# Kernel tuning notes

Measured on AMD Instinct MI355X. Metric: run time of the kernel, lower is better.

The kernel has to match this reference:

```python
import jax, jax.numpy as jnp
import numpy as np
from jax import lax

S = 262144   # sequence length (dim 2)
D = 16       # embedding width (dim 3)
L = 20       # number of conv layers
K_TOP = 800


def _conv(x, w, b, pad):
    # x: [B,C,H,W], w: [O,I,kh,1]; conv along H with symmetric padding, stride 1
    y = lax.conv_general_dilated(x, w, (1, 1), [(pad, pad), (0, 0)],
                                 dimension_numbers=('NCHW', 'OIHW', 'NCHW'))
    return y + b[None, :, None, None]


def _fold(x):
    # Faithful to the torch fold(): pairwise sum along width (dim 3), then the
    # buggy concatenation of C copies along dim 2 and B copies along dim 1.
    B, C, H, W = x.shape
    c = x[..., 0::2] + x[..., 1::2]          # [B,C,H,W//2]
    b = jnp.concatenate([c] * C, axis=2)      # [B,C,H*C,W//2]
    return jnp.concatenate([b] * B, axis=1)   # [B,C*B,H*C,W//2]


def _kmax(x, k):
    # torch k_max_pool returns top-k along dim 2 (H) for every width column
    # (the outer loops are dead code: it returns the last inner result `c`).
    xt = jnp.swapaxes(x, 2, 3)                # [B,C,W,H]
    v = lax.top_k(xt, k)[0]                   # [B,C,W,k] (descending)
    return jnp.swapaxes(v, 2, 3)              # [B,C,k,W]


def _prelu(x, a):
    return jnp.where(x >= 0, x, a * x)


def _forward(x, w0, b0, wm, bm, w18, b18, w19, b19, a1, a2, Wfc, bfc):
    s = x.shape[2]
    # layer 0: conv(99) -> fold -> kmax(max(k_top, s)) -> PReLU1
    h = _prelu(_kmax(_fold(_conv(x, w0, b0, 98)), max(K_TOP, s)), a1)
    # layers 1..17: conv(9) -> kmax -> PReLU2 (layer 1) / ReLU (layers 2..17)
    for i in range(17):
        k = max(K_TOP, int((L - 1 - i) / float(L) * s))
        h = _conv(h, wm[i], bm[i], 8)
        h = _kmax(h, k)
        h = _prelu(h, a2) if i == 0 else jax.nn.relu(h)
    # layer 18: conv(9) -> fold -> kmax -> ELU
    k18 = max(K_TOP, int((L - 18) / float(L) * s))
    h = jax.nn.elu(_kmax(_fold(_conv(h, w18, b18, 8)), k18))
    # layer 19: conv(358) -> fold -> kmax(k_top) -> ELU
    h = jax.nn.elu(_kmax(_fold(_conv(h, w19, b19, 357)), K_TOP))   # [1,5,800,2]
    h = h.reshape(-1, 2 * K_TOP)              # [5, 1600]
    h = h @ Wfc.T + bfc                        # dropout in eval = identity
    h = h.reshape(1, -1)                       # [1, 1000]; log_softmax dim=len(x)=1
    return jax.nn.log_softmax(h, axis=1)


def setup_inputs() -> dict:
    key = jax.random.key(0)
    ks = jax.random.split(key, 12)
    n = lambda k, sh, sc: jax.random.normal(k, sh, jnp.float32) * sc
    return {
        'x':   n(ks[0], (1, 1, S, D), 1.0),
        'w0':  n(ks[1], (2, 1, 99, 1), 0.05),  'b0':  n(ks[2], (2,), 0.05),
        'wm':  n(ks[3], (17, 2, 2, 9, 1), 0.2), 'bm': n(ks[4], (17, 2), 0.05),
        'w18': n(ks[5], (2, 2, 9, 1), 0.2),    'b18': n(ks[6], (2,), 0.05),
        'w19': n(ks[7], (5, 2, 358, 1), 0.03), 'b19': n(ks[8], (5,), 0.05),
        'a1': jnp.float32(0.25), 'a2': jnp.float32(0.25),
        'Wfc': n(ks[9], (200, 1600), 0.02),    'bfc': n(ks[10], (200,), 0.02),
    }


def reference(x, w0, b0, wm, bm, w18, b18, w19, b19, a1, a2, Wfc, bfc):
    return _forward(x, w0, b0, wm, bm, w18, b18, w19, b19, a1, a2, Wfc, bfc)
```

## Files before the change

### kernel.cpp

```cpp
#include <hip/hip_runtime.h>
#include <math.h>

typedef unsigned int u32;
typedef unsigned long long u64;

#define STRIDE 262656
#define KSHIFT 15
#define KROUND 0x4000u
#define BAND   6144
#define NB     12288
#define PA17   0x7100u
#define NA17   0x17700u
#define NCOLS  16
#define ZW     (NB*NCOLS)
#define ACT_PRELU 0
#define ACT_RELU  1
#define ACT_ELU   2

__device__ __forceinline__ float k2f(u32 k){
    u32 u = (k & 0x80000000u) ? k : (k ^ 0x7FFFFFFFu);
    return __uint_as_float(u);
}
__device__ __forceinline__ int bin_of(float v){
    float av = fabsf(v);
    av = fminf(fmaxf(av, 0.00390625f), 65535.96875f);
    u32 u = __float_as_uint(av);
    if (v < 0.f){
        u32 k = 0x80000000u | u;
        int b = (int)(((k + KROUND) >> KSHIFT) - NA17);
        b = b < 0 ? 0 : (b > BAND-1 ? BAND-1 : b);
        return BAND + b;
    } else {
        u32 k = u ^ 0x7FFFFFFFu;
        int b = (int)(((k + KROUND) >> KSHIFT) - PA17);
        b = b < 0 ? 0 : (b > BAND-1 ? BAND-1 : b);
        return b;
    }
}
__device__ __forceinline__ float bin_val(int bin){
    u32 k17 = (bin < BAND) ? ((u32)bin + PA17) : ((u32)(bin - BAND) + NA17);
    return k2f(k17 << KSHIFT);
}

__device__ __forceinline__ void hist_add(u32* __restrict__ Hc, int bin, bool valid, int lane){
    u32 bn = valid ? (u32)bin : 0xFFFFFFFFu;
    u32 prev = __shfl_up(bn, 1);
    bool diff = (lane == 0) || (prev != bn);
    u64 m = __ballot(diff || !valid);
    if (valid && diff){
        u64 above = m & ~((2ull << lane) - 1ull);
        int nxt = above ? (__ffsll((unsigned long long)above) - 1) : 64;
        atomicAdd(&Hc[bin], (u32)(nxt - lane));
    }
}

__device__ __forceinline__ void lds_hist_dedup(u32* __restrict__ hist, int bin, bool valid, int lane){
    u32 bn = valid ? (u32)bin : 0xFFFFFFFFu;
    u32 prev = __shfl_up(bn, 1);
    bool diff = (lane == 0) || (prev != bn);
    u64 m = __ballot(diff || !valid);
    if (valid && diff){
        u64 above = m & ~((2ull << lane) - 1ull);
        int nxt = above ? (__ffsll((unsigned long long)above) - 1) : 64;
        u32 cnt = (u32)(nxt - lane);
        atomicAdd(&hist[bin >> 1], cnt << ((bin & 1) * 16));
    }
}

__global__ __launch_bounds__(256) void foldx(const float* __restrict__ x, float* __restrict__ fx,
                                             uint4* __restrict__ zb)
{
    __shared__ float4 tile[1024];
    const int tid = threadIdx.x;
    const int h0 = blockIdx.x * 256;
    for (int i = tid; i < 1024; i += 256) tile[i] = ((const float4*)x)[(size_t)h0*4 + i];
    __syncthreads();
    float4 a = tile[tid*4+0], b = tile[tid*4+1], c = tile[tid*4+2], d = tile[tid*4+3];
    const int h = h0 + tid;
    fx[(size_t)0*STRIDE + h] = a.x + a.y;
    fx[(size_t)1*STRIDE + h] = a.z + a.w;
    fx[(size_t)2*STRIDE + h] = b.x + b.y;
    fx[(size_t)3*STRIDE + h] = b.z + b.w;
    fx[(size_t)4*STRIDE + h] = c.x + c.y;
    fx[(size_t)5*STRIDE + h] = c.z + c.w;
    fx[(size_t)6*STRIDE + h] = d.x + d.y;
    fx[(size_t)7*STRIDE + h] = d.z + d.w;
    const uint4 z = make_uint4(0,0,0,0);
    for (int i = blockIdx.x*256 + tid; i < ZW/4; i += gridDim.x*256) zb[i] = z;
}

#define C0CHUNK 8192
__global__ __launch_bounds__(512) void conv0_lds(const float* __restrict__ fx, u32* __restrict__ H,
                                                 const float* __restrict__ w0, const float* __restrict__ b0)
{
    __shared__ u32 hist[NB/2];
    __shared__ __align__(16) float s0f[2148];
    __shared__ float sw[100];
    const int colv = blockIdx.y;
    const int o = colv >> 3, wp = colv & 7;
    const int tid = threadIdx.x;
    const int p0 = blockIdx.x * C0CHUNK;
    const int p1 = min(p0 + C0CHUNK, 262242);
    if (p0 >= 262242) return;
    for (int i = tid; i < NB/2; i += 512) hist[i] = 0;
    if (tid < 99) sw[tid] = w0[o*99 + tid];
    if (tid == 99) sw[99] = 0.f;
    const float bias = 2.f * b0[o];
    __syncthreads();
    const float* fc = fx + (size_t)wp * STRIDE;
    const float4* s4 = (const float4*)s0f;
    for (int t0 = p0; t0 < p1; t0 += 2048){
        for (int i = tid; i < 2148; i += 512){
            int h = t0 - 98 + i;
            s0f[i] = (h >= 0 && h < 262144) ? fc[h] : 0.f;
        }
        __syncthreads();
        float a0 = bias, a1 = bias, a2 = bias, a3 = bias;
        float4 c = s4[tid];
        #pragma unroll
        for (int jb = 0; jb < 25; jb++){
            float4 n = s4[tid + jb + 1];
            float w0_ = sw[4*jb+0], w1_ = sw[4*jb+1], w2_ = sw[4*jb+2], w3_ = sw[4*jb+3];
            a0 += w0_*c.x; a1 += w0_*c.y; a2 += w0_*c.z; a3 += w0_*c.w;
            a0 += w1_*c.y; a1 += w1_*c.z; a2 += w1_*c.w; a3 += w1_*n.x;
            a0 += w2_*c.z; a1 += w2_*c.w; a2 += w2_*n.x; a3 += w2_*n.y;
            a0 += w3_*c.w; a1 += w3_*n.x; a2 += w3_*n.y; a3 += w3_*n.z;
            c = n;
        }
        int hp = t0 + tid*4;
        if (hp     < p1){ int b = bin_of(a0); atomicAdd(&hist[b>>1], 1u << ((b&1)*16)); }
        if (hp + 1 < p1){ int b = bin_of(a1); atomicAdd(&hist[b>>1], 1u << ((b&1)*16)); }
        if (hp + 2 < p1){ int b = bin_of(a2); atomicAdd(&hist[b>>1], 1u << ((b&1)*16)); }
        if (hp + 3 < p1){ int b = bin_of(a3); atomicAdd(&hist[b>>1], 1u << ((b&1)*16)); }
        __syncthreads();
    }
    u32* Hc = H + (size_t)colv * NB;
    for (int i = tid; i < NB/2; i += 512){
        u32 w = hist[i];
        if (w){
            u32 lo = w & 0xFFFFu, hi = w >> 16;
            if (lo) atomicAdd(&Hc[2*i],   lo);
            if (hi) atomicAdd(&Hc[2*i+1], hi);
        }
    }
}

#define C9CHUNK 8192
template<int FOLDIN>
__global__ __launch_bounds__(512) void conv9_lds(
    const float* __restrict__ In, u32* __restrict__ H,
    const float* __restrict__ Wt, const float* __restrict__ Bs,
    int Hin, int Hout, int Wi, int Wo, float bscale)
{
    __shared__ u32 hist[NB/2];
    __shared__ __align__(16) float s0f[2056];
    __shared__ __align__(16) float s1f[2056];
    const int colv = blockIdx.y;
    const int o = colv / Wo, wp = colv % Wo;
    const int tid = threadIdx.x;
    const int lane = tid & 63;
    const int p0 = blockIdx.x * C9CHUNK;
    const int p1 = min(p0 + C9CHUNK, Hout);
    if (p0 >= Hout) return;
    for (int i = tid; i < NB/2; i += 512) hist[i] = 0;
    float w0r[9], w1r[9];
    #pragma unroll
    for (int j = 0; j < 9; j++){ w0r[j] = Wt[(o*2)*9 + j]; w1r[j] = Wt[(o*2)*9 + 9 + j]; }
    const float bv = bscale * Bs[o];
    __syncthreads();
    const float* i00 = In + (size_t)(0*Wi + (FOLDIN ? 2*wp   : wp))*STRIDE;
    const float* i01 = In + (size_t)(0*Wi + (FOLDIN ? 2*wp+1 : wp))*STRIDE;
    const float* i10 = In + (size_t)(1*Wi + (FOLDIN ? 2*wp   : wp))*STRIDE;
    const float* i11 = In + (size_t)(1*Wi + (FOLDIN ? 2*wp+1 : wp))*STRIDE;
    const float4* s40 = (const float4*)s0f;
    const float4* s41 = (const float4*)s1f;
    for (int t0 = p0; t0 < p1; t0 += 2048){
        for (int i = tid; i < 2056; i += 512){
            int h = t0 - 8 + i;
            float v0 = 0.f, v1 = 0.f;
            if (h >= 0 && h < Hin){
                v0 = FOLDIN ? (i00[h] + i01[h]) : i00[h];
                v1 = FOLDIN ? (i10[h] + i11[h]) : i10[h];
            }
            s0f[i] = v0; s1f[i] = v1;
        }
        __syncthreads();
        float a0 = bv, a1 = bv, a2 = bv, a3 = bv;
        {
            float4 X = s40[tid], Y = s40[tid+1], Z = s40[tid+2];
            a0 += w0r[0]*X.x; a1 += w0r[0]*X.y; a2 += w0r[0]*X.z; a3 += w0r[0]*X.w;
            a0 += w0r[1]*X.y; a1 += w0r[1]*X.z; a2 += w0r[1]*X.w; a3 += w0r[1]*Y.x;
            a0 += w0r[2]*X.z; a1 += w0r[2]*X.w; a2 += w0r[2]*Y.x; a3 += w0r[2]*Y.y;
            a0 += w0r[3]*X.w; a1 += w0r[3]*Y.x; a2 += w0r[3]*Y.y; a3 += w0r[3]*Y.z;
            a0 += w0r[4]*Y.x; a1 += w0r[4]*Y.y; a2 += w0r[4]*Y.z; a3 += w0r[4]*Y.w;
            a0 += w0r[5]*Y.y; a1 += w0r[5]*Y.z; a2 += w0r[5]*Y.w; a3 += w0r[5]*Z.x;
            a0 += w0r[6]*Y.z; a1 += w0r[6]*Y.w; a2 += w0r[6]*Z.x; a3 += w0r[6]*Z.y;
            a0 += w0r[7]*Y.w; a1 += w0r[7]*Z.x; a2 += w0r[7]*Z.y; a3 += w0r[7]*Z.z;
            a0 += w0r[8]*Z.x; a1 += w0r[8]*Z.y; a2 += w0r[8]*Z.z; a3 += w0r[8]*Z.w;
        }
        {
            float4 X = s41[tid], Y = s41[tid+1], Z = s41[tid+2];
            a0 += w1r[0]*X.x; a1 += w1r[0]*X.y; a2 += w1r[0]*X.z; a3 += w1r[0]*X.w;
            a0 += w1r[1]*X.y; a1 += w1r[1]*X.z; a2 += w1r[1]*X.w; a3 += w1r[1]*Y.x;
            a0 += w1r[2]*X.z; a1 += w1r[2]*X.w; a2 += w1r[2]*Y.x; a3 += w1r[2]*Y.y;
            a0 += w1r[3]*X.w; a1 += w1r[3]*Y.x; a2 += w1r[3]*Y.y; a3 += w1r[3]*Y.z;
            a0 += w1r[4]*Y.x; a1 += w1r[4]*Y.y; a2 += w1r[4]*Y.z; a3 += w1r[4]*Y.w;
            a0 += w1r[5]*Y.y; a1 += w1r[5]*Y.z; a2 += w1r[5]*Y.w; a3 += w1r[5]*Z.x;
            a0 += w1r[6]*Y.z; a1 += w1r[6]*Y.w; a2 += w1r[6]*Z.x; a3 += w1r[6]*Z.y;
            a0 += w1r[7]*Y.w; a1 += w1r[7]*Z.x; a2 += w1r[7]*Z.y; a3 += w1r[7]*Z.z;
            a0 += w1r[8]*Z.x; a1 += w1r[8]*Z.y; a2 += w1r[8]*Z.z; a3 += w1r[8]*Z.w;
        }
        int hp = t0 + tid*4;
        lds_hist_dedup(hist, bin_of(a0), hp     < p1, lane);
        lds_hist_dedup(hist, bin_of(a1), hp + 1 < p1, lane);
        lds_hist_dedup(hist, bin_of(a2), hp + 2 < p1, lane);
        lds_hist_dedup(hist, bin_of(a3), hp + 3 < p1, lane);
        __syncthreads();
    }
    u32* Hc = H + (size_t)colv * NB;
    for (int i = tid; i < NB/2; i += 512){
        u32 w = hist[i];
        if (w){
            u32 lo = w & 0xFFFFu, hi = w >> 16;
            if (lo) atomicAdd(&Hc[2*i],   lo);
            if (hi) atomicAdd(&Hc[2*i+1], hi);
        }
    }
}

template<int INC, int OUTC>
__global__ __launch_bounds__(256) void conv_hist_t(
    const float* __restrict__ In, u32* __restrict__ H,
    const float* __restrict__ Wt, const float* __restrict__ Bs,
    int Hin, int Hout, int K, int pad, int Wi, int Wo, int foldIn, float bscale)
{
    __shared__ float sIn[INC][613];
    __shared__ float sW[OUTC*INC*358];
    const int wp = blockIdx.y;
    const int h0 = blockIdx.x * 256;
    const int tid = threadIdx.x;
    const int lane = tid & 63;
    const int tl = 256 + K - 1;
    for (int t = tid; t < INC*tl; t += 256){
        int c = t / tl, r = t - c*tl;
        int h = h0 - pad + r;
        float v = 0.f;
        if (h >= 0 && h < Hin){
            if (foldIn) v = In[(size_t)(c*Wi + 2*wp)*STRIDE + h] + In[(size_t)(c*Wi + 2*wp + 1)*STRIDE + h];
            else        v = In[(size_t)(c*Wi + wp)*STRIDE + h];
        }
        sIn[c][r] = v;
    }
    for (int t = tid; t < OUTC*INC*K; t += 256) sW[t] = Wt[t];
    __syncthreads();
    int hp = h0 + tid;
    bool valid = (hp < Hout);
    float acc[OUTC];
    #pragma unroll
    for (int o = 0; o < OUTC; o++) acc[o] = bscale * Bs[o];
    for (int c = 0; c < INC; c++){
        for (int j = 0; j < K; j++){
            float xv = sIn[c][tid + j];
            #pragma unroll
            for (int o = 0; o < OUTC; o++) acc[o] += sW[(o*INC + c)*K + j] * xv;
        }
    }
    #pragma unroll
    for (int o = 0; o < OUTC; o++)
        hist_add(H + (size_t)(o*Wo + wp)*NB, bin_of(acc[o]), valid, lane);
}

__global__ __launch_bounds__(1024) void scan_fill(
    const u32* __restrict__ H, float* __restrict__ dst, const float* __restrict__ alphaPtr,
    int kOut, int dup, int act, uint4* __restrict__ zb)
{
    __shared__ u32 pre[NB];
    __shared__ u32 warr[16];
    const int col = blockIdx.y;
    const int tid = threadIdx.x;
    const int lane = tid & 63, wv = tid >> 6;
    const u32* Hc = H + (size_t)col * NB;
    for (int i = tid; i < NB; i += 1024) pre[i] = Hc[i];
    __syncthreads();
    const int base = tid * 12;
    u32 v[12]; u32 s = 0;
    #pragma unroll
    for (int i = 0; i < 12; i++){ v[i] = pre[base + i]; s += v[i]; v[i] = s; }
    u32 ss = s;
    #pragma unroll
    for (int d = 1; d < 64; d <<= 1){
        u32 t = __shfl_up(ss, d);
        if (lane >= d) ss += t;
    }
    if (lane == 63) warr[wv] = ss;
    __syncthreads();
    u32 wb = 0;
    #pragma unroll
    for (int w = 0; w < 16; w++) wb += (w < wv) ? warr[w] : 0u;
    u32 excl = wb + ss - s;
    #pragma unroll
    for (int i = 0; i < 12; i++) pre[base + i] = v[i] + excl;
    __syncthreads();

    const int S  = gridDim.x;
    const int nr = kOut / dup;
    const int per = (nr + S*1024 - 1) / (S*1024);
    int i = (blockIdx.x*1024 + tid) * per;
    const int i1 = min(i + per, nr);
    float* d = dst + (size_t)col * STRIDE;
    const float alpha = alphaPtr[0];
    int lo0 = 0;
    while (i < i1){
        int lo = lo0, hi = NB - 1;
        while (lo < hi){ int m = (lo + hi) >> 1; if (pre[m] > (u32)i) hi = m; else lo = m + 1; }
        float vv = bin_val(lo);
        if (act == ACT_PRELU)      vv = (vv >= 0.f) ? vv : alpha * vv;
        else if (act == ACT_RELU)  vv = (vv > 0.f) ? vv : 0.f;
        else                       vv = (vv > 0.f) ? vv : expm1f(vv);
        int e = (int)min((u32)i1, pre[lo]);
        for (; i < e; i++){
            int bse = i * dup;
            for (int dd = 0; dd < dup; dd++) d[bse + dd] = vv;
        }
        lo0 = lo + 1;
    }
    const uint4 z = make_uint4(0,0,0,0);
    int lin = (blockIdx.y * gridDim.x + blockIdx.x) * 1024 + tid;
    int tot = gridDim.x * gridDim.y * 1024;
    for (int q = lin; q < ZW/4; q += tot) zb[q] = z;
}

__global__ __launch_bounds__(256) void fc_dot(const float* __restrict__ A, const float* __restrict__ Wfc,
                                              const float* __restrict__ bfc, float* __restrict__ logits)
{
    const int t = blockIdx.x;
    const int o = t / 200, j = t - o*200;
    const float* wrow = Wfc + (size_t)j*1600;
    float acc = 0.f;
    for (int q = threadIdx.x; q < 1600; q += 256){
        int p = q >> 1, wq = q & 1;
        acc += wrow[q] * A[(size_t)(o*2 + wq)*STRIDE + p];
    }
    __shared__ float red[256];
    red[threadIdx.x] = acc;
    __syncthreads();
    for (int s = 128; s > 0; s >>= 1){
        if (threadIdx.x < s) red[threadIdx.x] += red[threadIdx.x + s];
        __syncthreads();
    }
    if (threadIdx.x == 0) logits[t] = red[0] + bfc[j];
}

__global__ __launch_bounds__(1024) void lsm(const float* __restrict__ logits, float* __restrict__ out)
{
    const int tid = threadIdx.x;
    __shared__ float red[1024];
    float lg = (tid < 1000) ? logits[tid] : -INFINITY;
    red[tid] = lg;
    __syncthreads();
    for (int s = 512; s > 0; s >>= 1){
        if (tid < s) red[tid] = fmaxf(red[tid], red[tid + s]);
        __syncthreads();
    }
    float m = red[0];
    __syncthreads();
    red[tid] = (tid < 1000) ? expf(lg - m) : 0.f;
    __syncthreads();
    for (int s = 512; s > 0; s >>= 1){
        if (tid < s) red[tid] += red[tid + s];
        __syncthreads();
    }
    float lse = logf(red[0]);
    if (tid < 1000) out[tid] = lg - m - lse;
}

extern "C" void kernel_launch(void* const* d_in, const int* in_sizes, int n_in,
                              void* d_out, int out_size, void* d_ws, size_t ws_size,
                              hipStream_t stream)
{
    (void)in_sizes; (void)n_in; (void)out_size;
    const size_t need = (size_t)24*STRIDE*4 + (size_t)2*ZW*4 + 4096;
    if (ws_size < need) return;

    const float* x   = (const float*)d_in[0];
    const float* w0  = (const float*)d_in[1];
    const float* b0  = (const float*)d_in[2];
    const float* wm  = (const float*)d_in[3];
    const float* bm  = (const float*)d_in[4];
    const float* w18 = (const float*)d_in[5];
    const float* b18 = (const float*)d_in[6];
    const float* w19 = (const float*)d_in[7];
    const float* b19 = (const float*)d_in[8];
    const float* a1  = (const float*)d_in[9];
    const float* a2  = (const float*)d_in[10];
    const float* Wfc = (const float*)d_in[11];
    const float* bfc = (const float*)d_in[12];

    float* b1   = (float*)d_ws;
    float* fx   = b1 + (size_t)16*STRIDE;
    u32*  bin0  = (u32*)(fx + (size_t)8*STRIDE);
    u32*  bin1  = bin0 + (size_t)ZW;
    float* logits = (float*)(bin1 + (size_t)ZW);

    u32* cur = bin0;
    u32* nxt = bin1;

    foldx<<<1024, 256, 0, stream>>>(x, fx, (uint4*)cur);

    conv0_lds<<<dim3(33, 16), 512, 0, stream>>>(fx, cur, w0, b0);
    scan_fill<<<dim3(16, 16), 1024, 0, stream>>>(cur, b1, a1, 262144, 2, ACT_PRELU, (uint4*)nxt);
    { u32* t = cur; cur = nxt; nxt = t; }
    int Hin = 262144;

    static const int ks[17] = {249036,235929,222822,209715,196608,183500,170393,157286,
                               144179,131072,117964,104857,91750,78643,65536,52428,39321};
    for (int i = 0; i < 17; i++){
        int Hout = Hin + 8;
        int nch = (Hout + C9CHUNK - 1) / C9CHUNK;
        conv9_lds<0><<<dim3(nch, 16), 512, 0, stream>>>(
            b1, cur, wm + (size_t)i*36, bm + (size_t)i*2, Hin, Hout, 8, 8, 1.f);
        scan_fill<<<dim3(16, 16), 1024, 0, stream>>>(cur, b1, a2, ks[i], 1,
                                                     (i == 0) ? ACT_PRELU : ACT_RELU, (uint4*)nxt);
        { u32* t = cur; cur = nxt; nxt = t; }
        Hin = ks[i];
    }

    {
        int Hout = Hin + 8;
        int nch = (Hout + C9CHUNK - 1) / C9CHUNK;
        conv9_lds<1><<<dim3(nch, 8), 512, 0, stream>>>(
            b1, cur, w18, b18, Hin, Hout, 8, 4, 2.f);
        scan_fill<<<dim3(4, 8), 1024, 0, stream>>>(cur, b1, a2, 26214, 2, ACT_ELU, (uint4*)nxt);
        { u32* t = cur; cur = nxt; nxt = t; }
        Hin = 26214;
    }

    {
        int Hout = Hin + 714 - 358 + 1;
        conv_hist_t<2,5><<<dim3((Hout + 255)/256, 2), 256, 0, stream>>>(
            b1, cur, w19, b19, Hin, Hout, 358, 357, 4, 2, 1, 2.f);
        scan_fill<<<dim3(1, 10), 1024, 0, stream>>>(cur, b1, a2, 800, 5, ACT_ELU, (uint4*)nxt);
    }

    fc_dot<<<1000, 256, 0, stream>>>(b1, Wfc, bfc, logits);
    lsm<<<1, 1024, 0, stream>>>(logits, (float*)d_out);
}
```

Measured before the change: 726.9 us.

## Feed conv9 layers from histogram prefix sums instead of materialized sorted activations

For the 17 middle conv layers, scan_fill now writes only the per-column histogram prefix sums to global memory and skips writing the sorted activation arrays. A new runconv9 kernel rebuilds each input value on the fly by binary-searching the prefix array once per thread and then walking bins forward, applying the previous layer's activation. This removes the large global writes and reads of the sorted activation buffers between layers. In exchange it adds per-thread binary searches and divergent bin-walking loops, plus an extra workspace buffer.

```diff
diff --git a/kernel.cpp b/kernel.cpp
--- a/kernel.cpp
+++ b/kernel.cpp
@@ -41,6 +41,11 @@
     u32 k17 = (bin < BAND) ? ((u32)bin + PA17) : ((u32)(bin - BAND) + NA17);
     return k2f(k17 << KSHIFT);
 }
+__device__ __forceinline__ float actf(int act, float alpha, float v){
+    if (act == ACT_PRELU) return (v >= 0.f) ? v : alpha * v;
+    if (act == ACT_RELU)  return (v > 0.f) ? v : 0.f;
+    return (v > 0.f) ? v : expm1f(v);
+}
 
 __device__ __forceinline__ void hist_add(u32* __restrict__ Hc, int bin, bool valid, int lane){
     u32 bn = valid ? (u32)bin : 0xFFFFFFFFu;
@@ -146,6 +151,89 @@
 }
 
 #define C9CHUNK 8192
+__global__ __launch_bounds__(512) void runconv9(
+    const u32* __restrict__ P, u32* __restrict__ H,
+    const float* __restrict__ Wt, const float* __restrict__ Bs,
+    int Hin, int Hout, float bscale, int pact, const float* __restrict__ pAlpha, int pshift)
+{
+    __shared__ u32 hist[NB/2];
+    const int colv = blockIdx.y;
+    const int o = colv >> 3, wp = colv & 7;
+    const int tid = threadIdx.x;
+    const int lane = tid & 63;
+    const int p0 = blockIdx.x * C9CHUNK;
+    const int p1 = min(p0 + C9CHUNK, Hout);
+    if (p0 >= Hout) return;
+    for (int i = tid; i < NB/2; i += 512) hist[i] = 0;
+    float w0r[9], w1r[9];
+    #pragma unroll
+    for (int j = 0; j < 9; j++){ w0r[j] = Wt[(o*2)*9 + j]; w1r[j] = Wt[(o*2)*9 + 9 + j]; }
+    const float bv = bscale * Bs[o];
+    const float pal = pAlpha[0];
+    __syncthreads();
+    const u32* P0 = P + (size_t)(0*8 + wp)*NB;
+    const u32* P1 = P + (size_t)(1*8 + wp)*NB;
+    const int start = p0 + tid*16;
+
+    int b0, b1i; u32 e0, e1; float v0c, v1c;
+    {
+        int rr = start - 8; if (rr < 0) rr = 0; if (rr >= Hin) rr = Hin - 1;
+        u32 r = (u32)(rr >> pshift);
+        int lo = 0, hi = NB - 1;
+        while (lo < hi){ int m = (lo+hi)>>1; if (P0[m] > r) hi = m; else lo = m + 1; }
+        b0 = lo; e0 = P0[lo]; v0c = actf(pact, pal, bin_val(lo));
+        lo = 0; hi = NB - 1;
+        while (lo < hi){ int m = (lo+hi)>>1; if (P1[m] > r) hi = m; else lo = m + 1; }
+        b1i = lo; e1 = P1[lo]; v1c = actf(pact, pal, bin_val(lo));
+    }
+    float win0[8], win1[8];
+    #pragma unroll
+    for (int k = 0; k < 8; k++){
+        int h = start - 8 + k;
+        float v0 = 0.f, v1 = 0.f;
+        if (h >= 0 && h < Hin){
+            u32 r = (u32)(h >> pshift);
+            while (e0 <= r){ ++b0; e0 = P0[b0]; v0c = actf(pact, pal, bin_val(b0)); }
+            while (e1 <= r){ ++b1i; e1 = P1[b1i]; v1c = actf(pact, pal, bin_val(b1i)); }
+            v0 = v0c; v1 = v1c;
+        }
+        win0[k] = v0; win1[k] = v1;
+    }
+    #pragma unroll
+    for (int q = 0; q < 16; q++){
+        int hp = start + q;
+        float nv0 = 0.f, nv1 = 0.f;
+        if (hp < Hin){
+            u32 r = (u32)(hp >> pshift);
+            while (e0 <= r){ ++b0; e0 = P0[b0]; v0c = actf(pact, pal, bin_val(b0)); }
+            while (e1 <= r){ ++b1i; e1 = P1[b1i]; v1c = actf(pact, pal, bin_val(b1i)); }
+            nv0 = v0c; nv1 = v1c;
+        }
+        float a = bv;
+        a += w0r[0]*win0[0]; a += w0r[1]*win0[1]; a += w0r[2]*win0[2]; a += w0r[3]*win0[3];
+        a += w0r[4]*win0[4]; a += w0r[5]*win0[5]; a += w0r[6]*win0[6]; a += w0r[7]*win0[7];
+        a += w0r[8]*nv0;
+        a += w1r[0]*win1[0]; a += w1r[1]*win1[1]; a += w1r[2]*win1[2]; a += w1r[3]*win1[3];
+        a += w1r[4]*win1[4]; a += w1r[5]*win1[5]; a += w1r[6]*win1[6]; a += w1r[7]*win1[7];
+        a += w1r[8]*nv1;
+        bool valid = (hp < p1) && (start < p1);
+        lds_hist_dedup(hist, bin_of(a), valid, lane);
+        #pragma unroll
+        for (int k = 0; k < 7; k++){ win0[k] = win0[k+1]; win1[k] = win1[k+1]; }
+        win0[7] = nv0; win1[7] = nv1;
+    }
+    __syncthreads();
+    u32* Hc = H + (size_t)colv * NB;
+    for (int i = tid; i < NB/2; i += 512){
+        u32 w = hist[i];
+        if (w){
+            u32 lo = w & 0xFFFFu, hi = w >> 16;
+            if (lo) atomicAdd(&Hc[2*i],   lo);
+            if (hi) atomicAdd(&Hc[2*i+1], hi);
+        }
+    }
+}
+
 template<int FOLDIN>
 __global__ __launch_bounds__(512) void conv9_lds(
     const float* __restrict__ In, u32* __restrict__ H,
@@ -272,7 +360,8 @@
 
 __global__ __launch_bounds__(1024) void scan_fill(
     const u32* __restrict__ H, float* __restrict__ dst, const float* __restrict__ alphaPtr,
-    int kOut, int dup, int act, uint4* __restrict__ zb)
+    int kOut, int dup, int act, int fill, int pref, u32* __restrict__ prefOut,
+    uint4* __restrict__ zb)
 {
     __shared__ u32 pre[NB];
     __shared__ u32 warr[16];
@@ -302,27 +391,33 @@
     for (int i = 0; i < 12; i++) pre[base + i] = v[i] + excl;
     __syncthreads();
 
-    const int S  = gridDim.x;
-    const int nr = kOut / dup;
-    const int per = (nr + S*1024 - 1) / (S*1024);
-    int i = (blockIdx.x*1024 + tid) * per;
-    const int i1 = min(i + per, nr);
-    float* d = dst + (size_t)col * STRIDE;
-    const float alpha = alphaPtr[0];
-    int lo0 = 0;
-    while (i < i1){
-        int lo = lo0, hi = NB - 1;
-        while (lo < hi){ int m = (lo + hi) >> 1; if (pre[m] > (u32)i) hi = m; else lo = m + 1; }
-        float vv = bin_val(lo);
-        if (act == ACT_PRELU)      vv = (vv >= 0.f) ? vv : alpha * vv;
-        else if (act == ACT_RELU)  vv = (vv > 0.f) ? vv : 0.f;
-        else                       vv = (vv > 0.f) ? vv : expm1f(vv);
-        int e = (int)min((u32)i1, pre[lo]);
-        for (; i < e; i++){
-            int bse = i * dup;
-            for (int dd = 0; dd < dup; dd++) d[bse + dd] = vv;
-        }
-        lo0 = lo + 1;
+    if (pref && blockIdx.x == 0){
+        u32* po = prefOut + (size_t)col * NB;
+        for (int i = tid; i < NB; i += 1024) po[i] = pre[i];
+    }
+    if (fill){
+        const int S  = gridDim.x;
+        const int nr = kOut / dup;
+        const int per = (nr + S*1024 - 1) / (S*1024);
+        int i = (blockIdx.x*1024 + tid) * per;
+        const int i1 = min(i + per, nr);
+        float* d = dst + (size_t)col * STRIDE;
+        const float alpha = alphaPtr[0];
+        int lo0 = 0;
+        while (i < i1){
+            int lo = lo0, hi = NB - 1;
+            while (lo < hi){ int m = (lo + hi) >> 1; if (pre[m] > (u32)i) hi = m; else lo = m + 1; }
+            float vv = bin_val(lo);
+            if (act == ACT_PRELU)      vv = (vv >= 0.f) ? vv : alpha * vv;
+            else if (act == ACT_RELU)  vv = (vv > 0.f) ? vv : 0.f;
+            else                       vv = (vv > 0.f) ? vv : expm1f(vv);
+            int e = (int)min((u32)i1, pre[lo]);
+            for (; i < e; i++){
+                int bse = i * dup;
+                for (int dd = 0; dd < dup; dd++) d[bse + dd] = vv;
+            }
+            lo0 = lo + 1;
+        }
     }
     const uint4 z = make_uint4(0,0,0,0);
     int lin = (blockIdx.y * gridDim.x + blockIdx.x) * 1024 + tid;
@@ -379,7 +474,7 @@
                               hipStream_t stream)
 {
     (void)in_sizes; (void)n_in; (void)out_size;
-    const size_t need = (size_t)24*STRIDE*4 + (size_t)2*ZW*4 + 4096;
+    const size_t need = (size_t)24*STRIDE*4 + (size_t)3*ZW*4 + 8192;
     if (ws_size < need) return;
 
     const float* x   = (const float*)d_in[0];
@@ -400,7 +495,8 @@
     float* fx   = b1 + (size_t)16*STRIDE;
     u32*  bin0  = (u32*)(fx + (size_t)8*STRIDE);
     u32*  bin1  = bin0 + (size_t)ZW;
-    float* logits = (float*)(bin1 + (size_t)ZW);
+    u32*  preG  = bin1 + (size_t)ZW;
+    float* logits = (float*)(preG + (size_t)ZW);
 
     u32* cur = bin0;
     u32* nxt = bin1;
@@ -408,7 +504,8 @@
     foldx<<<1024, 256, 0, stream>>>(x, fx, (uint4*)cur);
 
     conv0_lds<<<dim3(33, 16), 512, 0, stream>>>(fx, cur, w0, b0);
-    scan_fill<<<dim3(16, 16), 1024, 0, stream>>>(cur, b1, a1, 262144, 2, ACT_PRELU, (uint4*)nxt);
+    scan_fill<<<dim3(16, 16), 1024, 0, stream>>>(cur, b1, a1, 262144, 2, ACT_PRELU,
+                                                 0, 1, preG, (uint4*)nxt);
     { u32* t = cur; cur = nxt; nxt = t; }
     int Hin = 262144;
 
@@ -417,10 +514,15 @@
     for (int i = 0; i < 17; i++){
         int Hout = Hin + 8;
         int nch = (Hout + C9CHUNK - 1) / C9CHUNK;
-        conv9_lds<0><<<dim3(nch, 16), 512, 0, stream>>>(
-            b1, cur, wm + (size_t)i*36, bm + (size_t)i*2, Hin, Hout, 8, 8, 1.f);
+        int pact = (i == 0) ? ACT_PRELU : (i == 1) ? ACT_PRELU : ACT_RELU;
+        const float* palpha = (i == 0) ? a1 : a2;
+        int pshift = (i == 0) ? 1 : 0;
+        runconv9<<<dim3(nch, 16), 512, 0, stream>>>(
+            preG, cur, wm + (size_t)i*36, bm + (size_t)i*2, Hin, Hout, 1.f, pact, palpha, pshift);
+        int isLast = (i == 16);
         scan_fill<<<dim3(16, 16), 1024, 0, stream>>>(cur, b1, a2, ks[i], 1,
-                                                     (i == 0) ? ACT_PRELU : ACT_RELU, (uint4*)nxt);
+                                                     (i == 0) ? ACT_PRELU : ACT_RELU,
+                                                     isLast ? 1 : 0, isLast ? 0 : 1, preG, (uint4*)nxt);
         { u32* t = cur; cur = nxt; nxt = t; }
         Hin = ks[i];
     }
@@ -430,7 +532,8 @@
         int nch = (Hout + C9CHUNK - 1) / C9CHUNK;
         conv9_lds<1><<<dim3(nch, 8), 512, 0, stream>>>(
             b1, cur, w18, b18, Hin, Hout, 8, 4, 2.f);
-        scan_fill<<<dim3(4, 8), 1024, 0, stream>>>(cur, b1, a2, 26214, 2, ACT_ELU, (uint4*)nxt);
+        scan_fill<<<dim3(4, 8), 1024, 0, stream>>>(cur, b1, a2, 26214, 2, ACT_ELU,
+                                                   1, 0, preG, (uint4*)nxt);
         { u32* t = cur; cur = nxt; nxt = t; }
         Hin = 26214;
     }
@@ -439,7 +542,8 @@
         int Hout = Hin + 714 - 358 + 1;
         conv_hist_t<2,5><<<dim3((Hout + 255)/256, 2), 256, 0, stream>>>(
             b1, cur, w19, b19, Hin, Hout, 358, 357, 4, 2, 1, 2.f);
-        scan_fill<<<dim3(1, 10), 1024, 0, stream>>>(cur, b1, a2, 800, 5, ACT_ELU, (uint4*)nxt);
+        scan_fill<<<dim3(1, 10), 1024, 0, stream>>>(cur, b1, a2, 800, 5, ACT_ELU,
+                                                    1, 0, preG, (uint4*)nxt);
     }
 
     fc_dot<<<1000, 256, 0, stream>>>(b1, Wfc, bfc, logits);
```

Result: slower. 2.740 ms (+276.9%).
